# Performance work log

Measured on AMD Instinct MI355X. Metric: run time of the kernel, lower is better.

Reference implementation:

```python
import jax, jax.numpy as jnp
import numpy as np

B, S, E, A = 4, 2048, 1024, 64  # batch, seq, embedding_size, attention_size


def setup_inputs() -> dict:
    key = jax.random.key(0)
    k1, k2 = jax.random.split(key)
    embedding = jax.random.normal(k1, (B, S, E), dtype=jnp.float32)
    # nn.Linear(embedding_size, attention_size, bias=False).weight has shape [A, E]
    Wk = jax.random.normal(k2, (A, E), dtype=jnp.float32) * (1.0 / np.sqrt(E))
    return {"embedding": embedding, "Wk": Wk}


def reference(embedding, Wk):
    # NOTE: the original module (buggily) calls self.key() for q, k, AND v.
    # We reproduce that math faithfully: q = k = v = embedding @ Wk.T.
    k = jnp.einsum('bse,ae->bsa', embedding, Wk)  # [B,S,A]
    q = k
    v = k
    x = jnp.einsum('bqa,bka->bqk', q, k) / jnp.sqrt(jnp.float32(A))  # [B,S,S]
    # Faithful to masked_fill(torch.tril(x) == 0, -inf): masks the strict upper
    # triangle (tril zeros it) plus any lower-triangle entries exactly equal to 0.
    x = jnp.where(jnp.tril(x) == 0, -jnp.inf, x)
    x = jax.nn.softmax(x, axis=2)
    return jnp.einsum('bqk,bka->bqa', x, v)  # [B,S,A]
```

## Files before the change

### kernel.cpp

```cpp
#include <hip/hip_runtime.h>
#include <math.h>

#define BATCH 4
#define SLEN  2048
#define EMB   1024
#define AH    64

typedef __attribute__((ext_vector_type(8))) short bf16x8;
typedef __attribute__((ext_vector_type(4))) float f32x4;

#define MFMA16(a, b, c) __builtin_amdgcn_mfma_f32_16x16x32_bf16((a), (b), (c), 0, 0, 0)

__device__ __forceinline__ void async16(const void* g, void* l) {
  __builtin_amdgcn_global_load_lds(
      (const __attribute__((address_space(1))) unsigned int*)g,
      (__attribute__((address_space(3))) unsigned int*)l, 16, 0, 0);
}

__device__ __forceinline__ short f2bf(float x) {
  union { float f; unsigned u; } v; v.f = x;
  unsigned r = v.u + 0x7fffu + ((v.u >> 16) & 1u);
  return (short)(r >> 16);
}
__device__ __forceinline__ float bf2f(short h) {
  union { unsigned u; float f; } v; v.u = ((unsigned)(unsigned short)h) << 16;
  return v.f;
}

__device__ __forceinline__ void split_trunc(float4 a0, float4 a1, bf16x8& hi, bf16x8& lo) {
  unsigned c[8] = {__float_as_uint(a0.x), __float_as_uint(a0.y), __float_as_uint(a0.z),
                   __float_as_uint(a0.w), __float_as_uint(a1.x), __float_as_uint(a1.y),
                   __float_as_uint(a1.z), __float_as_uint(a1.w)};
  union { bf16x8 v; unsigned d[4]; } H, L;
  H.d[0] = __builtin_amdgcn_perm(c[1], c[0], 0x07060302u);
  H.d[1] = __builtin_amdgcn_perm(c[3], c[2], 0x07060302u);
  H.d[2] = __builtin_amdgcn_perm(c[5], c[4], 0x07060302u);
  H.d[3] = __builtin_amdgcn_perm(c[7], c[6], 0x07060302u);
  unsigned e[8];
#pragma unroll
  for (int j = 0; j < 8; ++j)
    e[j] = __float_as_uint(__uint_as_float(c[j]) - __uint_as_float(c[j] & 0xffff0000u));
  L.d[0] = __builtin_amdgcn_perm(e[1], e[0], 0x07060302u);
  L.d[1] = __builtin_amdgcn_perm(e[3], e[2], 0x07060302u);
  L.d[2] = __builtin_amdgcn_perm(e[5], e[4], 0x07060302u);
  L.d[3] = __builtin_amdgcn_perm(e[7], e[6], 0x07060302u);
  hi = H.v; lo = L.v;
}

__device__ __forceinline__ int slot_off(int qt) {
  return (qt == 0) ? 0 : qt + (((qt - 1) * (qt - 1)) >> 2);
}

#define CH_SHORTS 24576

__global__ __launch_bounds__(256) void prep_wk_kernel(const float* __restrict__ Wk,
                                                      short* __restrict__ BpkG) {
  int tg = blockIdx.x * 256 + threadIdx.x;
  int kc = tg >> 8, rem = tg & 255, nt = rem >> 6, lane = rem & 63;
  int n = nt * 16 + (lane & 15);
  int k = kc * 32 + (lane >> 4) * 8;
  const float* src = Wk + (size_t)n * EMB + k;
  float4 a0 = *(const float4*)src;
  float4 a1 = *(const float4*)(src + 4);
  bf16x8 hi, lo;
  split_trunc(a0, a1, hi, lo);
  short* dst = BpkG + ((size_t)(kc * 4 + nt) * 128 + lane) * 8;
  *(bf16x8*)dst = hi;
  *(bf16x8*)(dst + 512) = lo;
}

__global__ __launch_bounds__(256) void gemm_k_kernel(const float* __restrict__ emb,
                                                     const short* __restrict__ BpkG,
                                                     short* __restrict__ Kpack) {
  __shared__ __align__(16) char glds[40960];
  float* embT = (float*)glds;
  short* bpkT = (short*)(glds + 8192);

  const int t = threadIdx.x;
  const int w = t >> 6, l = t & 63, lm = l & 15, quad = l >> 4;
  const int nt = w;
  const int row0 = blockIdx.x * 16;

  f32x4 acc = {0.f, 0.f, 0.f, 0.f};

  for (int step = 0; step < 8; ++step) {
    __syncthreads();
#pragma unroll
    for (int u = 0; u < 2; ++u) {
      int rowl = (w * 2 + u) * 2 + (l >> 5);
      int du = (l & 31) ^ (rowl & 7);
      async16(emb + (size_t)(row0 + rowl) * EMB + step * 128 + du * 4,
              embT + (w * 2 + u) * 256);
    }
    const short* bg = BpkG + (size_t)step * 16384;
#pragma unroll
    for (int u = 0; u < 8; ++u)
      async16(bg + (w * 8 + u) * 512 + l * 8, bpkT + (w * 8 + u) * 512);
    __syncthreads();

#pragma unroll
    for (int kc = 0; kc < 4; ++kc) {
      int du0 = kc * 8 + quad * 2;
      float4 a0 = *(const float4*)((char*)embT + lm * 512 + ((du0) ^ (lm & 7)) * 16);
      float4 a1 = *(const float4*)((char*)embT + lm * 512 + ((du0 + 1) ^ (lm & 7)) * 16);
      bf16x8 ahi, alo;
      split_trunc(a0, a1, ahi, alo);
      bf16x8 bhi = *(const bf16x8*)(bpkT + (((kc * 4 + nt) * 2 + 0) * 64 + l) * 8);
      bf16x8 blo = *(const bf16x8*)(bpkT + (((kc * 4 + nt) * 2 + 1) * 64 + l) * 8);
      acc = MFMA16(ahi, bhi, acc);
      acc = MFMA16(ahi, blo, acc);
      acc = MFMA16(alo, bhi, acc);
    }
  }

  const int a = nt * 16 + lm;
#pragma unroll
  for (int r = 0; r < 4; ++r) {
    int srow = row0 + quad * 4 + r;
    float v = acc[r];
    short h = f2bf(v);
    short lo2 = f2bf(v - bf2f(h));
    int bb = srow >> 11, si = srow & 2047, c = si >> 7, key = si & 127;
    int kb = key >> 4, klm = key & 15;
    size_t cb = (size_t)(bb * 16 + c) * CH_SHORTS;
    size_t kbo = (size_t)((kb * 2 + (a >> 5)) * 64 + ((a & 31) >> 3) * 16 + klm) * 8 + (a & 7);
    Kpack[cb + kbo] = h;
    Kpack[cb + 8192 + kbo] = lo2;
    size_t vbo = (size_t)(((key >> 5) * 4 + (a >> 4)) * 64 + ((key & 31) >> 3) * 16 + (a & 15)) * 8 + (key & 7);
    Kpack[cb + 16384 + vbo] = h;
  }
}

__global__ __launch_bounds__(256) void flash_kernel(const short* __restrict__ Kpack,
                                                    short* __restrict__ OpartH,
                                                    float2* __restrict__ mlpart) {
  const int chunk = blockIdx.x, qt = blockIdx.y, b = blockIdx.z;
  if (2 * chunk > qt) return;

  __shared__ __align__(16) short KLs[CH_SHORTS];
  const int t = threadIdx.x;
  const int w = t >> 6, l = t & 63, lm = l & 15, quad = l >> 4;
  const int qr0 = qt * 64 + w * 16, k0 = chunk * 128;

  const short* qG = Kpack + (size_t)(b * 16 + (qt >> 1)) * CH_SHORTS + ((qt & 1) * 4 + w) * 1024;
  bf16x8 qh0 = *(const bf16x8*)(qG + l * 8);
  bf16x8 qh1 = *(const bf16x8*)(qG + 512 + l * 8);
  bf16x8 ql0 = *(const bf16x8*)(qG + 8192 + l * 8);
  bf16x8 ql1 = *(const bf16x8*)(qG + 8192 + 512 + l * 8);

  const short* chunkG = Kpack + (size_t)(b * 16 + chunk) * CH_SHORTS;
#pragma unroll
  for (int u = 0; u < 12; ++u) {
    int slot = w * 12 + u;
    async16(chunkG + slot * 512 + l * 8, KLs + slot * 512);
  }
  __syncthreads();

  f32x4 sc[8];
#pragma unroll
  for (int g = 0; g < 8; ++g) {
    bf16x8 bh0 = *(const bf16x8*)(KLs + ((g * 2 + 0) * 64 + l) * 8);
    bf16x8 bh1 = *(const bf16x8*)(KLs + ((g * 2 + 1) * 64 + l) * 8);
    bf16x8 bl0 = *(const bf16x8*)(KLs + 8192 + ((g * 2 + 0) * 64 + l) * 8);
    bf16x8 bl1 = *(const bf16x8*)(KLs + 8192 + ((g * 2 + 1) * 64 + l) * 8);
    f32x4 s = {0.f, 0.f, 0.f, 0.f};
    s = MFMA16(qh0, bh0, s);
    s = MFMA16(qh0, bl0, s);
    s = MFMA16(ql0, bh0, s);
    s = MFMA16(qh1, bh1, s);
    s = MFMA16(qh1, bl1, s);
    s = MFMA16(ql1, bh1, s);
    sc[g] = s;
  }

  float rm[4] = {-INFINITY, -INFINITY, -INFINITY, -INFINITY};
#pragma unroll
  for (int g = 0; g < 8; ++g) {
    const int col = k0 + g * 16 + lm;
#pragma unroll
    for (int r = 0; r < 4; ++r) {
      const int row = qr0 + quad * 4 + r;
      float v = sc[g][r] * 0.125f;
      v = (col > row || v == 0.0f) ? -INFINITY : v;
      sc[g][r] = v;
      rm[r] = fmaxf(rm[r], v);
    }
  }
  float m_i[4], l_i[4];
#pragma unroll
  for (int r = 0; r < 4; ++r) {
    for (int off = 1; off < 16; off <<= 1) rm[r] = fmaxf(rm[r], __shfl_xor(rm[r], off, 16));
    m_i[r] = rm[r];
  }
  float rs[4] = {0.f, 0.f, 0.f, 0.f};
#pragma unroll
  for (int g = 0; g < 8; ++g)
#pragma unroll
    for (int r = 0; r < 4; ++r) {
      float p = (sc[g][r] == -INFINITY) ? 0.f : __expf(sc[g][r] - m_i[r]);
      sc[g][r] = p;
      rs[r] += p;
    }
#pragma unroll
  for (int r = 0; r < 4; ++r) {
    for (int off = 1; off < 16; off <<= 1) rs[r] += __shfl_xor(rs[r], off, 16);
    l_i[r] = rs[r];
  }

  __syncthreads();

  short* Pw = KLs + w * 2112;
#pragma unroll
  for (int g = 0; g < 8; ++g)
#pragma unroll
    for (int r = 0; r < 4; ++r)
      Pw[(quad * 4 + r) * 132 + g * 16 + lm] = f2bf(sc[g][r]);

  f32x4 o[4] = {{0.f,0.f,0.f,0.f},{0.f,0.f,0.f,0.f},{0.f,0.f,0.f,0.f},{0.f,0.f,0.f,0.f}};
#pragma unroll
  for (int kc2 = 0; kc2 < 4; ++kc2) {
    bf16x8 pf = *(const bf16x8*)(Pw + lm * 132 + kc2 * 32 + quad * 8);
#pragma unroll
    for (int nt = 0; nt < 4; ++nt) {
      bf16x8 vf = *(const bf16x8*)(KLs + 16384 + ((kc2 * 4 + nt) * 64 + l) * 8);
      o[nt] = MFMA16(pf, vf, o[nt]);
    }
  }

  const int slot = b * 272 + slot_off(qt) + chunk;
  short* Ob = OpartH + (size_t)slot * 4096;
#pragma unroll
  for (int nt = 0; nt < 4; ++nt)
#pragma unroll
    for (int r = 0; r < 4; ++r)
      Ob[(size_t)(w * 16 + quad * 4 + r) * AH + nt * 16 + lm] = f2bf(o[nt][r]);
  if (lm == 0) {
#pragma unroll
    for (int r = 0; r < 4; ++r)
      mlpart[(size_t)slot * 64 + w * 16 + quad * 4 + r] = make_float2(m_i[r], l_i[r]);
  }
}

__global__ __launch_bounds__(256) void merge_kernel(const short* __restrict__ OpartH,
                                                    const float2* __restrict__ mlpart,
                                                    float* __restrict__ out) {
  __shared__ __align__(16) short ldsO[16 * 1024];
  __shared__ float wtab[16][17];
  const int t = threadIdx.x;
  const int w = t >> 6, l = t & 63;
  const int rg = blockIdx.x, qt = blockIdx.y, b = blockIdx.z;
  const int r0 = rg * 16;
  const int nch = (qt >> 1) + 1;
  const int slotbase = b * 272 + slot_off(qt);

#pragma unroll
  for (int u = 0; u < 8; ++u) {
    int idx = w * 8 + u;
    int c = idx >> 1, half = idx & 1;
    if (c < nch)
      async16(OpartH + (size_t)(slotbase + c) * 4096 + r0 * 64 + half * 512 + l * 8,
              ldsO + c * 1024 + half * 512 + l * 8);
  }

  const int row = w * 4 + (l >> 4), c = l & 15;
  float mc = -INFINITY, lc = 0.f;
  if (c < nch) {
    float2 ml = mlpart[(size_t)(slotbase + c) * 64 + r0 + row];
    mc = ml.x; lc = ml.y;
  }
  float M = mc;
  for (int off = 1; off < 16; off <<= 1) M = fmaxf(M, __shfl_xor(M, off, 16));
  float wgt = (mc != -INFINITY) ? __expf(mc - M) : 0.f;
  float L = lc * wgt;
  for (int off = 1; off < 16; off <<= 1) L += __shfl_xor(L, off, 16);
  wtab[row][c] = wgt / L;

  __syncthreads();

  const int row2 = t >> 4, a0 = (t & 15) * 4;
  float4 acc = make_float4(0.f, 0.f, 0.f, 0.f);
  for (int cc = 0; cc < nch; ++cc) {
    float wv = wtab[row2][cc];
    short4 v4 = *(const short4*)(ldsO + cc * 1024 + row2 * 64 + a0);
    acc.x += wv * bf2f(v4.x); acc.y += wv * bf2f(v4.y);
    acc.z += wv * bf2f(v4.z); acc.w += wv * bf2f(v4.w);
  }
  *(float4*)&out[((size_t)(b * 2048 + qt * 64 + r0 + row2)) * AH + a0] = acc;
}

extern "C" void kernel_launch(void* const* d_in, const int* in_sizes, int n_in,
                              void* d_out, int out_size, void* d_ws, size_t ws_size,
                              hipStream_t stream) {
  const float* emb = (const float*)d_in[0];
  const float* Wk  = (const float*)d_in[1];
  float* out = (float*)d_out;
  char* ws = (char*)d_ws;

  short*  Kpack  = (short*)(ws);
  short*  BpkG   = (short*)(ws + 3145728);
  short*  OpartH = (short*)(ws + 3670016);
  float2* mlpart = (float2*)(ws + 12582912);

  prep_wk_kernel<<<dim3(32), dim3(256), 0, stream>>>(Wk, BpkG);
  gemm_k_kernel<<<dim3(512), dim3(256), 0, stream>>>(emb, BpkG, Kpack);
  flash_kernel<<<dim3(16, 32, 4), dim3(256), 0, stream>>>(Kpack, OpartH, mlpart);
  merge_kernel<<<dim3(4, 32, 4), dim3(256), 0, stream>>>(OpartH, mlpart, out);
}
```

Measured before the change: 109.3 us.

## Double-buffer K-projection GEMM and reuse K/V chunk across two query tiles

Result: no change. 110.9 us (+1.4%).

```diff
diff --git a/kernel.cpp b/kernel.cpp
--- a/kernel.cpp
+++ b/kernel.cpp
@@ -73,40 +73,43 @@
                                                      const short* __restrict__ BpkG,
                                                      short* __restrict__ Kpack) {
   __shared__ __align__(16) char glds[40960];
-  float* embT = (float*)glds;
-  short* bpkT = (short*)(glds + 8192);
 
   const int t = threadIdx.x;
   const int w = t >> 6, l = t & 63, lm = l & 15, quad = l >> 4;
   const int nt = w;
   const int row0 = blockIdx.x * 16;
 
+  auto stage = [&](int step, int bs) {
+    char* base = glds + bs * 20480;
+    float* eT = (float*)base;
+    short* bT = (short*)(base + 4096);
+    int rowl = 4 * w + (l >> 4);
+    int du = (l & 15) ^ (rowl & 7);
+    async16(emb + (size_t)(row0 + rowl) * EMB + step * 64 + du * 4, eT + w * 256);
+    const short* bg = BpkG + (size_t)step * 8192;
+#pragma unroll
+    for (int u = 0; u < 4; ++u)
+      async16(bg + (w * 4 + u) * 512 + l * 8, bT + (w * 4 + u) * 512);
+  };
+
   f32x4 acc = {0.f, 0.f, 0.f, 0.f};
-
-  for (int step = 0; step < 8; ++step) {
+  stage(0, 0);
+#pragma unroll
+  for (int s = 0; s < 16; ++s) {
     __syncthreads();
-#pragma unroll
-    for (int u = 0; u < 2; ++u) {
-      int rowl = (w * 2 + u) * 2 + (l >> 5);
-      int du = (l & 31) ^ (rowl & 7);
-      async16(emb + (size_t)(row0 + rowl) * EMB + step * 128 + du * 4,
-              embT + (w * 2 + u) * 256);
-    }
-    const short* bg = BpkG + (size_t)step * 16384;
-#pragma unroll
-    for (int u = 0; u < 8; ++u)
-      async16(bg + (w * 8 + u) * 512 + l * 8, bpkT + (w * 8 + u) * 512);
-    __syncthreads();
-
-#pragma unroll
-    for (int kc = 0; kc < 4; ++kc) {
+    if (s < 15) stage(s + 1, (s + 1) & 1);
+    char* base = glds + (s & 1) * 20480;
+    float* eT = (float*)base;
+    short* bT = (short*)(base + 4096);
+#pragma unroll
+    for (int kc = 0; kc < 2; ++kc) {
       int du0 = kc * 8 + quad * 2;
-      float4 a0 = *(const float4*)((char*)embT + lm * 512 + ((du0) ^ (lm & 7)) * 16);
-      float4 a1 = *(const float4*)((char*)embT + lm * 512 + ((du0 + 1) ^ (lm & 7)) * 16);
+      float4 a0 = *(const float4*)((char*)eT + lm * 256 + ((du0) ^ (lm & 7)) * 16);
+      float4 a1 = *(const float4*)((char*)eT + lm * 256 + ((du0 + 1) ^ (lm & 7)) * 16);
       bf16x8 ahi, alo;
       split_trunc(a0, a1, ahi, alo);
-      bf16x8 bhi = *(const bf16x8*)(bpkT + (((kc * 4 + nt) * 2 + 0) * 64 + l) * 8);
-      bf16x8 blo = *(const bf16x8*)(bpkT + (((kc * 4 + nt) * 2 + 1) * 64 + l) * 8);
+      bf16x8 bhi = *(const bf16x8*)(bT + (((kc * 4 + nt) * 2 + 0) * 64 + l) * 8);
+      bf16x8 blo = *(const bf16x8*)(bT + (((kc * 4 + nt) * 2 + 1) * 64 + l) * 8);
       acc = MFMA16(ahi, bhi, acc);
       acc = MFMA16(ahi, blo, acc);
       acc = MFMA16(alo, bhi, acc);
@@ -131,113 +134,129 @@
   }
 }
 
-__global__ __launch_bounds__(256) void flash_kernel(const short* __restrict__ Kpack,
-                                                    short* __restrict__ OpartH,
-                                                    float2* __restrict__ mlpart) {
-  const int chunk = blockIdx.x, qt = blockIdx.y, b = blockIdx.z;
-  if (2 * chunk > qt) return;
-
-  __shared__ __align__(16) short KLs[CH_SHORTS];
+__global__ __launch_bounds__(256, 3) void flash_kernel(const short* __restrict__ Kpack,
+                                                       short* __restrict__ OpartH,
+                                                       float2* __restrict__ mlpart) {
+  const int c = blockIdx.x, g = blockIdx.y, b = blockIdx.z;
+  if (c > g) return;
+
+  __shared__ __align__(16) short KLs[16384];
+  __shared__ __align__(16) short Plds[4][16][132];
+
   const int t = threadIdx.x;
   const int w = t >> 6, l = t & 63, lm = l & 15, quad = l >> 4;
-  const int qr0 = qt * 64 + w * 16, k0 = chunk * 128;
-
-  const short* qG = Kpack + (size_t)(b * 16 + (qt >> 1)) * CH_SHORTS + ((qt & 1) * 4 + w) * 1024;
-  bf16x8 qh0 = *(const bf16x8*)(qG + l * 8);
-  bf16x8 qh1 = *(const bf16x8*)(qG + 512 + l * 8);
-  bf16x8 ql0 = *(const bf16x8*)(qG + 8192 + l * 8);
-  bf16x8 ql1 = *(const bf16x8*)(qG + 8192 + 512 + l * 8);
-
-  const short* chunkG = Kpack + (size_t)(b * 16 + chunk) * CH_SHORTS;
-#pragma unroll
-  for (int u = 0; u < 12; ++u) {
-    int slot = w * 12 + u;
+  const int k0 = c * 128;
+
+  const short* chunkG = Kpack + (size_t)(b * 16 + c) * CH_SHORTS;
+#pragma unroll
+  for (int u = 0; u < 8; ++u) {
+    int slot = w * 8 + u;
     async16(chunkG + slot * 512 + l * 8, KLs + slot * 512);
   }
+
+  const short* qGb = Kpack + (size_t)(b * 16 + g) * CH_SHORTS;
+  bf16x8 qh0[2], qh1[2], ql0[2], ql1[2];
+#pragma unroll
+  for (int qi = 0; qi < 2; ++qi) {
+    const short* qG = qGb + (qi * 4 + w) * 1024;
+    qh0[qi] = *(const bf16x8*)(qG + l * 8);
+    qh1[qi] = *(const bf16x8*)(qG + 512 + l * 8);
+    ql0[qi] = *(const bf16x8*)(qG + 8192 + l * 8);
+    ql1[qi] = *(const bf16x8*)(qG + 8192 + 512 + l * 8);
+  }
+
+  bf16x8 vf[4][4];
+#pragma unroll
+  for (int kc2 = 0; kc2 < 4; ++kc2)
+#pragma unroll
+    for (int nt = 0; nt < 4; ++nt)
+      vf[kc2][nt] = *(const bf16x8*)(chunkG + 16384 + ((kc2 * 4 + nt) * 64 + l) * 8);
+
   __syncthreads();
 
-  f32x4 sc[8];
-#pragma unroll
-  for (int g = 0; g < 8; ++g) {
-    bf16x8 bh0 = *(const bf16x8*)(KLs + ((g * 2 + 0) * 64 + l) * 8);
-    bf16x8 bh1 = *(const bf16x8*)(KLs + ((g * 2 + 1) * 64 + l) * 8);
-    bf16x8 bl0 = *(const bf16x8*)(KLs + 8192 + ((g * 2 + 0) * 64 + l) * 8);
-    bf16x8 bl1 = *(const bf16x8*)(KLs + 8192 + ((g * 2 + 1) * 64 + l) * 8);
-    f32x4 s = {0.f, 0.f, 0.f, 0.f};
-    s = MFMA16(qh0, bh0, s);
-    s = MFMA16(qh0, bl0, s);
-    s = MFMA16(ql0, bh0, s);
-    s = MFMA16(qh1, bh1, s);
-    s = MFMA16(qh1, bl1, s);
-    s = MFMA16(ql1, bh1, s);
-    sc[g] = s;
-  }
-
-  float rm[4] = {-INFINITY, -INFINITY, -INFINITY, -INFINITY};
-#pragma unroll
-  for (int g = 0; g < 8; ++g) {
-    const int col = k0 + g * 16 + lm;
+#pragma unroll
+  for (int qi = 0; qi < 2; ++qi) {
+    const int qt = 2 * g + qi;
+    const int qr0 = qt * 64 + w * 16;
+
+    f32x4 sc[8];
+#pragma unroll
+    for (int kg = 0; kg < 8; ++kg) {
+      bf16x8 bh0 = *(const bf16x8*)(KLs + ((kg * 2 + 0) * 64 + l) * 8);
+      bf16x8 bh1 = *(const bf16x8*)(KLs + ((kg * 2 + 1) * 64 + l) * 8);
+      bf16x8 bl0 = *(const bf16x8*)(KLs + 8192 + ((kg * 2 + 0) * 64 + l) * 8);
+      bf16x8 bl1 = *(const bf16x8*)(KLs + 8192 + ((kg * 2 + 1) * 64 + l) * 8);
+      f32x4 s = {0.f, 0.f, 0.f, 0.f};
+      s = MFMA16(qh0[qi], bh0, s);
+      s = MFMA16(qh0[qi], bl0, s);
+      s = MFMA16(ql0[qi], bh0, s);
+      s = MFMA16(qh1[qi], bh1, s);
+      s = MFMA16(qh1[qi], bl1, s);
+      s = MFMA16(ql1[qi], bh1, s);
+      sc[kg] = s;
+    }
+
+    float rm[4] = {-INFINITY, -INFINITY, -INFINITY, -INFINITY};
+#pragma unroll
+    for (int kg = 0; kg < 8; ++kg) {
+      const int col = k0 + kg * 16 + lm;
+#pragma unroll
+      for (int r = 0; r < 4; ++r) {
+        const int row = qr0 + quad * 4 + r;
+        float v = sc[kg][r] * 0.125f;
+        v = (col > row || v == 0.0f) ? -INFINITY : v;
+        sc[kg][r] = v;
+        rm[r] = fmaxf(rm[r], v);
+      }
+    }
+    float m_i[4], l_i[4];
 #pragma unroll
     for (int r = 0; r < 4; ++r) {
-      const int row = qr0 + quad * 4 + r;
-      float v = sc[g][r] * 0.125f;
-      v = (col > row || v == 0.0f) ? -INFINITY : v;
-      sc[g][r] = v;
-      rm[r] = fmaxf(rm[r], v);
-    }
-  }
-  float m_i[4], l_i[4];
-#pragma unroll
-  for (int r = 0; r < 4; ++r) {
-    for (int off = 1; off < 16; off <<= 1) rm[r] = fmaxf(rm[r], __shfl_xor(rm[r], off, 16));
-    m_i[r] = rm[r];
-  }
-  float rs[4] = {0.f, 0.f, 0.f, 0.f};
-#pragma unroll
-  for (int g = 0; g < 8; ++g)
+      for (int off = 1; off < 16; off <<= 1) rm[r] = fmaxf(rm[r], __shfl_xor(rm[r], off, 16));
+      m_i[r] = rm[r];
+    }
+    float rs[4] = {0.f, 0.f, 0.f, 0.f};
+#pragma unroll
+    for (int kg = 0; kg < 8; ++kg)
+#pragma unroll
+      for (int r = 0; r < 4; ++r) {
+        float p = (sc[kg][r] == -INFINITY) ? 0.f : __expf(sc[kg][r] - m_i[r]);
+        sc[kg][r] = p;
+        rs[r] += p;
+      }
 #pragma unroll
     for (int r = 0; r < 4; ++r) {
-      float p = (sc[g][r] == -INFINITY) ? 0.f : __expf(sc[g][r] - m_i[r]);
-      sc[g][r] = p;
-      rs[r] += p;
-    }
-#pragma unroll
-  for (int r = 0; r < 4; ++r) {
-    for (int off = 1; off < 16; off <<= 1) rs[r] += __shfl_xor(rs[r], off, 16);
-    l_i[r] = rs[r];
-  }
-
-  __syncthreads();
-
-  short* Pw = KLs + w * 2112;
-#pragma unroll
-  for (int g = 0; g < 8; ++g)
-#pragma unroll
-    for (int r = 0; r < 4; ++r)
-      Pw[(quad * 4 + r) * 132 + g * 16 + lm] = f2bf(sc[g][r]);
-
-  f32x4 o[4] = {{0.f,0.f,0.f,0.f},{0.f,0.f,0.f,0.f},{0.f,0.f,0.f,0.f},{0.f,0.f,0.f,0.f}};
-#pragma unroll
-  for (int kc2 = 0; kc2 < 4; ++kc2) {
-    bf16x8 pf = *(const bf16x8*)(Pw + lm * 132 + kc2 * 32 + quad * 8);
-#pragma unroll
-    for (int nt = 0; nt < 4; ++nt) {
-      bf16x8 vf = *(const bf16x8*)(KLs + 16384 + ((kc2 * 4 + nt) * 64 + l) * 8);
-      o[nt] = MFMA16(pf, vf, o[nt]);
-    }
-  }
-
-  const int slot = b * 272 + slot_off(qt) + chunk;
-  short* Ob = OpartH + (size_t)slot * 4096;
-#pragma unroll
-  for (int nt = 0; nt < 4; ++nt)
-#pragma unroll
-    for (int r = 0; r < 4; ++r)
-      Ob[(size_t)(w * 16 + quad * 4 + r) * AH + nt * 16 + lm] = f2bf(o[nt][r]);
-  if (lm == 0) {
-#pragma unroll
-    for (int r = 0; r < 4; ++r)
-      mlpart[(size_t)slot * 64 + w * 16 + quad * 4 + r] = make_float2(m_i[r], l_i[r]);
+      for (int off = 1; off < 16; off <<= 1) rs[r] += __shfl_xor(rs[r], off, 16);
+      l_i[r] = rs[r];
+    }
+
+#pragma unroll
+    for (int kg = 0; kg < 8; ++kg)
+#pragma unroll
+      for (int r = 0; r < 4; ++r)
+        Plds[w][quad * 4 + r][kg * 16 + lm] = f2bf(sc[kg][r]);
+
+    f32x4 o[4] = {{0.f,0.f,0.f,0.f},{0.f,0.f,0.f,0.f},{0.f,0.f,0.f,0.f},{0.f,0.f,0.f,0.f}};
+#pragma unroll
+    for (int kc2 = 0; kc2 < 4; ++kc2) {
+      bf16x8 pf = *(const bf16x8*)&Plds[w][lm][kc2 * 32 + quad * 8];
+#pragma unroll
+      for (int nt = 0; nt < 4; ++nt)
+        o[nt] = MFMA16(pf, vf[kc2][nt], o[nt]);
+    }
+
+    const int slot = b * 272 + slot_off(qt) + c;
+    short* Ob = OpartH + (size_t)slot * 4096;
+#pragma unroll
+    for (int nt = 0; nt < 4; ++nt)
+#pragma unroll
+      for (int r = 0; r < 4; ++r)
+        Ob[(size_t)(w * 16 + quad * 4 + r) * AH + nt * 16 + lm] = f2bf(o[nt][r]);
+    if (lm == 0) {
+#pragma unroll
+      for (int r = 0; r < 4; ++r)
+        mlpart[(size_t)slot * 64 + w * 16 + quad * 4 + r] = make_float2(m_i[r], l_i[r]);
+    }
   }
 }
 
@@ -303,6 +322,6 @@
 
   prep_wk_kernel<<<dim3(32), dim3(256), 0, stream>>>(Wk, BpkG);
   gemm_k_kernel<<<dim3(512), dim3(256), 0, stream>>>(emb, BpkG, Kpack);
-  flash_kernel<<<dim3(16, 32, 4), dim3(256), 0, stream>>>(Kpack, OpartH, mlpart);
+  flash_kernel<<<dim3(16, 16, 4), dim3(256), 0, stream>>>(Kpack, OpartH, mlpart);
   merge_kernel<<<dim3(4, 32, 4), dim3(256), 0, stream>>>(OpartH, mlpart, out);
 }
```
